# Kernel optimization log

Hardware: AMD Instinct MI355X
Metric: run time of the kernel (lower is better)

Reference implementation:

```python
import jax, jax.numpy as jnp
import numpy as np

B, DIM, H, W = 1, 48, 128, 128
NH = 1  # num_heads; original broadcasting only valid for num_heads == 1


def setup_inputs() -> dict:
    key = jax.random.key(0)
    ks = jax.random.split(key, 5)
    x = jax.random.normal(ks[0], (B, DIM, H, W), jnp.float32)
    # 1x1 conv weights stored as [out, in] matrices (bias=False)
    qkv_w = jax.random.normal(ks[1], (3 * DIM, DIM), jnp.float32) * 0.05
    # depthwise 3x3 conv weight, groups = 3*DIM -> [3*DIM, 1, 3, 3]
    dw_w = jax.random.normal(ks[2], (3 * DIM, 1, 3, 3), jnp.float32) * 0.05
    proj_w = jax.random.normal(ks[3], (DIM, DIM), jnp.float32) * 0.05
    temperature = jnp.ones((NH, 1, 1), jnp.float32)
    return {"x": x, "qkv_w": qkv_w, "dw_w": dw_w, "proj_w": proj_w,
            "temperature": temperature}


def _l2norm(t, eps=1e-12):
    # F.normalize(dim=-1): x / max(||x||_2, eps)
    n = jnp.sqrt(jnp.sum(t * t, axis=-1, keepdims=True))
    return t / jnp.maximum(n, eps)


def reference(x, qkv_w, dw_w, proj_w, temperature):
    b, c, h, w = x.shape
    # qkv 1x1 conv (pointwise) then 3x3 depthwise conv
    qkv = jnp.einsum('bchw,oc->bohw', x, qkv_w)
    qkv = jax.lax.conv_general_dilated(
        qkv, dw_w, window_strides=(1, 1), padding='SAME',
        feature_group_count=3 * c,
        dimension_numbers=('NCHW', 'OIHW', 'NCHW'))
    q, k, v = jnp.split(qkv, 3, axis=1)  # each [b, c, h, w]
    # b c h w -> b (h w) c
    tok = lambda t: t.reshape(b, c, h * w).transpose(0, 2, 1)
    q, k, v = tok(q), tok(k), tok(v)
    q = _l2norm(q)
    k = _l2norm(k)
    # full (hw x hw) cosine attention with learned temperature (scalar, NH=1)
    attn = jnp.einsum('bnc,bmc->bnm', q, k) * temperature  # [b, hw, hw]
    attn = jax.nn.softmax(attn, axis=-1)
    out = jnp.einsum('bnm,bmc->bnc', attn, v)  # [b, hw, c]
    out = out.transpose(0, 2, 1).reshape(b, c, h, w)
    return jnp.einsum('bchw,oc->bohw', out, proj_w)
```

## Files before the change

### kernel.cpp

```cpp
#include <hip/hip_runtime.h>
#include <hip/hip_bf16.h>

#define NPIX 16384
#define NC   48

typedef __attribute__((ext_vector_type(16))) float f32x16;
typedef __attribute__((ext_vector_type(8))) short short8v;
typedef __attribute__((ext_vector_type(8))) unsigned short ushort8v;
typedef __attribute__((ext_vector_type(2))) unsigned int uint2v;

static __device__ __forceinline__ unsigned short f2bf(float x) {
  union { float f; unsigned u; } v; v.f = x;
  unsigned r = v.u + 0x7fffu + ((v.u >> 16) & 1u);
  return (unsigned short)(r >> 16);
}
static __device__ __forceinline__ float bf2f(unsigned short b) {
  union { unsigned u; float f; } v; v.u = ((unsigned)b) << 16;
  return v.f;
}

__global__ __launch_bounds__(256) void k_qkv(const float* __restrict__ in,
                                             const float* __restrict__ w,
                                             unsigned short* __restrict__ out) {
  int p = blockIdx.x * 256 + threadIdx.x;
  int og = blockIdx.y * 16;
  __shared__ float wl[16][NC];
  for (int i = threadIdx.x; i < 16 * NC; i += 256)
    wl[i / NC][i % NC] = w[(og + i / NC) * NC + i % NC];
  __syncthreads();
  float acc[16];
#pragma unroll
  for (int j = 0; j < 16; ++j) acc[j] = 0.f;
  for (int c = 0; c < NC; ++c) {
    float xv = in[c * NPIX + p];
#pragma unroll
    for (int j = 0; j < 16; ++j) acc[j] += xv * wl[j][c];
  }
#pragma unroll
  for (int j = 0; j < 16; ++j) out[(og + j) * NPIX + p] = f2bf(acc[j]);
}

__global__ __launch_bounds__(256) void k_dwconv(const unsigned short* __restrict__ in,
                                                const float* __restrict__ w,
                                                unsigned short* __restrict__ out) {
  __shared__ unsigned short srows[18][136];
  const int o = blockIdx.y;
  const int by = blockIdx.x;
  const int tid = threadIdx.x;
  const float* wt = w + o * 9;
  for (int idx = tid; idx < 288; idx += 256) {
    int r = idx >> 4, cx = idx & 15;
    int gy = by * 16 + r - 1;
    ushort8v vv = {0, 0, 0, 0, 0, 0, 0, 0};
    if (gy >= 0 && gy < 128)
      vv = *(const ushort8v*)(in + o * NPIX + gy * 128 + cx * 8);
    *(ushort8v*)&srows[r][cx * 8] = vv;
  }
  __syncthreads();
  const int r = tid >> 4;
  const int x0 = (tid & 15) * 8;
  float row[3][10];
#pragma unroll
  for (int dy = 0; dy < 3; ++dy) {
    int lr = r + dy;
    ushort8v mid = *(const ushort8v*)&srows[lr][x0];
#pragma unroll
    for (int j = 0; j < 8; ++j) row[dy][j + 1] = bf2f(mid[j]);
    row[dy][0] = (x0 > 0) ? bf2f(srows[lr][x0 - 1]) : 0.f;
    row[dy][9] = (x0 + 8 < 128) ? bf2f(srows[lr][x0 + 8]) : 0.f;
  }
  float wv[9];
#pragma unroll
  for (int i = 0; i < 9; ++i) wv[i] = wt[i];
  unsigned short res[8];
#pragma unroll
  for (int j = 0; j < 8; ++j) {
    float acc = 0.f;
#pragma unroll
    for (int dy = 0; dy < 3; ++dy)
#pragma unroll
      for (int dx = 0; dx < 3; ++dx)
        acc += wv[dy * 3 + dx] * row[dy][j + dx];
    res[j] = f2bf(acc);
  }
  int gy = by * 16 + r;
  *(ushort8v*)(out + o * NPIX + gy * 128 + x0) = *(ushort8v*)res;
}

__global__ __launch_bounds__(128) void k_norm(const unsigned short* __restrict__ dwqb,
                                              const float* __restrict__ temp,
                                              unsigned short* __restrict__ qn,
                                              unsigned short* __restrict__ kn) {
  const int tid = threadIdx.x;
  const int p = blockIdx.x * 64 + (tid & 63);
  const int half = tid >> 6;
  float t = temp[0] * 1.44269504088896f;
  const unsigned short* src = dwqb + half * 48 * NPIX;
  float v[48];
  float sq = 0.f;
#pragma unroll
  for (int c = 0; c < 48; ++c) {
    v[c] = bf2f(src[c * NPIX + p]);
    sq += v[c] * v[c];
  }
  float scale = (half == 0 ? t : 1.f) / fmaxf(sqrtf(sq), 1e-12f);
  unsigned short ob[48];
#pragma unroll
  for (int c = 0; c < 48; ++c) ob[c] = f2bf(v[c] * scale);
  unsigned short* dst = (half == 0 ? qn : kn) + p * 48;
#pragma unroll
  for (int j = 0; j < 6; ++j)
    *(ushort8v*)(dst + j * 8) = *(ushort8v*)&ob[j * 8];
}

__global__ __launch_bounds__(256) void k_attn8(const unsigned short* __restrict__ qn,
                                               const unsigned short* __restrict__ kn,
                                               const unsigned short* __restrict__ vb,
                                               float* __restrict__ numS) {
  __shared__ __align__(16) char smem[57344];
  const int tid = threadIdx.x;
  const int lane = tid & 63, wid = tid >> 6;
  const int l31 = lane & 31, lh = lane >> 5;
  const int bidx = blockIdx.x;
  const int ks = bidx & 7;
  const int qb = bidx >> 3;
  const int qbase = qb * 128 + wid * 32;

  short8v qf[3];
#pragma unroll
  for (int s = 0; s < 3; ++s)
    qf[s] = *(const short8v*)(qn + (qbase + l31) * 48 + s * 16 + lh * 8);

  f32x16 acc[2];
#pragma unroll
  for (int b = 0; b < 2; ++b)
#pragma unroll
    for (int r = 0; r < 16; ++r) acc[b][r] = 0.f;

  int kgoff[3], kloff[3], vgoff[3], vloff[3];
#pragma unroll
  for (int i = 0; i < 3; ++i) {
    int chunk = tid + 256 * i;
    int key = chunk / 6, part = chunk - key * 6;
    kgoff[i] = key * 48 + part * 8;
    kloff[i] = (key * 96 + part * 16) ^ ((key & 7) << 4);
    int c2 = chunk >> 4, kp = chunk & 15;
    vgoff[i] = c2 * NPIX + kp * 8;
    vloff[i] = 12288 + ((c2 * 256 + kp * 16) ^ ((c2 & 15) << 4));
  }

  for (int i = tid; i < 512; i += 256) {
    int b = i >> 8, j = i & 255;
    int c = 48 + (j >> 4), kp = j & 15;
    unsigned short val = (c == 48) ? (unsigned short)0x3F80 : (unsigned short)0;
    ushort8v vv = {val, val, val, val, val, val, val, val};
    *(ushort8v*)(smem + b * 28672 + 12288 + ((c * 256 + kp * 16) ^ ((c & 15) << 4))) = vv;
  }
  {
    const int m0 = ks * 2048;
#pragma unroll
    for (int i = 0; i < 3; ++i) {
      *(short8v*)(smem + kloff[i]) = *(const short8v*)(kn + m0 * 48 + kgoff[i]);
      *(short8v*)(smem + vloff[i]) = *(const short8v*)(vb + m0 + vgoff[i]);
    }
  }
  __syncthreads();

  for (int t = 0; t < 16; ++t) {
    char* buf = smem + (t & 1) * 28672;
    char* nbuf = smem + ((t + 1) & 1) * 28672;
    short8v pfk[3], pfv[3];
    const bool hasNext = (t + 1 < 16);
    if (hasNext) {
      const int m0n = ks * 2048 + (t + 1) * 128;
#pragma unroll
      for (int i = 0; i < 3; ++i) {
        pfk[i] = *(const short8v*)(kn + m0n * 48 + kgoff[i]);
        pfv[i] = *(const short8v*)(vb + m0n + vgoff[i]);
      }
    }
#pragma unroll
    for (int kb = 0; kb < 128; kb += 32) {
      f32x16 sacc;
#pragma unroll
      for (int r = 0; r < 16; ++r) sacc[r] = 0.f;
      int key = kb + l31;
#pragma unroll
      for (int s = 0; s < 3; ++s) {
        short8v kf = *(const short8v*)(buf +
            ((key * 96 + s * 32 + lh * 16) ^ ((key & 7) << 4)));
        sacc = __builtin_amdgcn_mfma_f32_32x32x16_bf16(kf, qf[s], sacc, 0, 0, 0);
      }
      float p[16];
#pragma unroll
      for (int r = 0; r < 16; ++r) p[r] = __builtin_amdgcn_exp2f(sacc[r]);
#pragma unroll
      for (int h = 0; h < 2; ++h) {
        unsigned a0, a1, b0, b1;
        asm("v_cvt_pk_bf16_f32 %0, %1, %2" : "=v"(a0) : "v"(p[8 * h + 0]), "v"(p[8 * h + 1]));
        asm("v_cvt_pk_bf16_f32 %0, %1, %2" : "=v"(a1) : "v"(p[8 * h + 2]), "v"(p[8 * h + 3]));
        asm("v_cvt_pk_bf16_f32 %0, %1, %2" : "=v"(b0) : "v"(p[8 * h + 4]), "v"(p[8 * h + 5]));
        asm("v_cvt_pk_bf16_f32 %0, %1, %2" : "=v"(b1) : "v"(p[8 * h + 6]), "v"(p[8 * h + 7]));
        uint2v s0 = __builtin_amdgcn_permlane32_swap(a0, b0, false, false);
        uint2v s1 = __builtin_amdgcn_permlane32_swap(a1, b1, false, false);
        union { unsigned u[4]; short8v v; } pa;
        pa.u[0] = s0[0]; pa.u[1] = s1[0]; pa.u[2] = s0[1]; pa.u[3] = s1[1];
        int kbase = kb + 16 * h + 8 * lh;
        short8v vf0 = *(const short8v*)(buf + 12288 +
            ((l31 * 256 + kbase * 2) ^ ((l31 & 15) << 4)));
        acc[0] = __builtin_amdgcn_mfma_f32_32x32x16_bf16(pa.v, vf0, acc[0], 0, 0, 0);
        int c1 = 32 + l31;
        short8v vf1 = *(const short8v*)(buf + 12288 +
            ((c1 * 256 + kbase * 2) ^ ((c1 & 15) << 4)));
        acc[1] = __builtin_amdgcn_mfma_f32_32x32x16_bf16(pa.v, vf1, acc[1], 0, 0, 0);
      }
    }
    if (hasNext) {
#pragma unroll
      for (int i = 0; i < 3; ++i) {
        *(short8v*)(nbuf + kloff[i]) = pfk[i];
        *(short8v*)(nbuf + vloff[i]) = pfv[i];
      }
    }
    __syncthreads();
  }

  __syncthreads();
  float* ot = (float*)smem + wid * (32 * 52);
#pragma unroll
  for (int r = 0; r < 16; ++r) {
    int q = (r & 3) + 8 * (r >> 2) + 4 * lh;
    ot[q * 52 + l31] = acc[0][r];
    if (l31 < 17) ot[q * 52 + 32 + l31] = acc[1][r];
  }
  __syncthreads();
  for (int idx = lane; idx < 49 * 32; idx += 64) {
    int q = idx & 31, c = idx >> 5;
    atomicAdd(&numS[(c << 14) + qbase + q], ot[q * 52 + c]);
  }
}

__global__ __launch_bounds__(256) void k_proj(const float* __restrict__ numS,
                                              const float* __restrict__ w,
                                              float* __restrict__ out) {
  __shared__ float wl[48][48];
  __shared__ float tok[48][64];
  __shared__ float dinv[64];
  const int t = threadIdx.x;
  const int px = t & 63, grp = t >> 6;
  const int p0 = blockIdx.x * 64;
  for (int i = t; i < 48 * 48; i += 256) wl[i / 48][i % 48] = w[i];
#pragma unroll
  for (int i = 0; i < 12; ++i) {
    int c = grp * 12 + i;
    tok[c][px] = numS[(c << 14) + p0 + px];
  }
  if (grp == 0) dinv[px] = 1.f / numS[(48 << 14) + p0 + px];
  __syncthreads();
  float rd = dinv[px];
#pragma unroll
  for (int i = 0; i < 12; ++i) {
    int o = grp * 12 + i;
    float a = 0.f;
#pragma unroll
    for (int c = 0; c < 48; ++c) a += wl[o][c] * tok[c][px];
    out[o * NPIX + p0 + px] = a * rd;
  }
}

extern "C" void kernel_launch(void* const* d_in, const int* in_sizes, int n_in,
                              void* d_out, int out_size, void* d_ws, size_t ws_size,
                              hipStream_t stream) {
  const float* x      = (const float*)d_in[0];
  const float* qkv_w  = (const float*)d_in[1];
  const float* dw_w   = (const float*)d_in[2];
  const float* proj_w = (const float*)d_in[3];
  const float* temp   = (const float*)d_in[4];

  char* wsb = (char*)d_ws;
  unsigned short* qn   = (unsigned short*)wsb;
  unsigned short* kn   = (unsigned short*)(wsb + 1572864);
  unsigned short* dwqb = (unsigned short*)(wsb + 3145728);
  unsigned short* vb   = dwqb + 96 * NPIX;
  unsigned short* qkvb = (unsigned short*)(wsb + 7864320);
  float* numS = (float*)(wsb + 7864320);

  k_qkv<<<dim3(64, 9), 256, 0, stream>>>(x, qkv_w, qkvb);
  k_dwconv<<<dim3(8, 144), 256, 0, stream>>>(qkvb, dw_w, dwqb);
  k_norm<<<dim3(256), 128, 0, stream>>>(dwqb, temp, qn, kn);
  hipMemsetAsync(numS, 0, (size_t)49 * NPIX * 4, stream);
  k_attn8<<<dim3(1024), 256, 0, stream>>>(qn, kn, vb, numS);
  k_proj<<<dim3(256), 256, 0, stream>>>(numS, proj_w, (float*)d_out);
}
```

Before: 120.6 us.

## Double attention block to 512 threads so K/V tiles serve 256 queries

The attention kernel now runs 512-thread blocks covering 256 queries (8 waves) instead of 128, with half as many blocks. Each staged K/V tile in shared memory is reused by twice as many query waves, halving global K/V traffic per query. The load work is redistributed so each thread moves three chunks, some from K and some from V. The cost is fewer blocks in flight (512 over the CUs), larger per-block synchronisation, and possibly lower occupancy.

```diff
diff --git a/kernel.cpp b/kernel.cpp
--- a/kernel.cpp
+++ b/kernel.cpp
@@ -113,7 +113,7 @@
     *(ushort8v*)(dst + j * 8) = *(ushort8v*)&ob[j * 8];
 }
 
-__global__ __launch_bounds__(256) void k_attn8(const unsigned short* __restrict__ qn,
+__global__ __launch_bounds__(512) void k_attn8(const unsigned short* __restrict__ qn,
                                                const unsigned short* __restrict__ kn,
                                                const unsigned short* __restrict__ vb,
                                                float* __restrict__ numS) {
@@ -124,7 +124,7 @@
   const int bidx = blockIdx.x;
   const int ks = bidx & 7;
   const int qb = bidx >> 3;
-  const int qbase = qb * 128 + wid * 32;
+  const int qbase = qb * 256 + wid * 32;
 
   short8v qf[3];
 #pragma unroll
@@ -137,20 +137,27 @@
 #pragma unroll
     for (int r = 0; r < 16; ++r) acc[b][r] = 0.f;
 
-  int kgoff[3], kloff[3], vgoff[3], vloff[3];
+  int goff[3], loff[3];
+  bool isK[3];
 #pragma unroll
   for (int i = 0; i < 3; ++i) {
-    int chunk = tid + 256 * i;
-    int key = chunk / 6, part = chunk - key * 6;
-    kgoff[i] = key * 48 + part * 8;
-    kloff[i] = (key * 96 + part * 16) ^ ((key & 7) << 4);
-    int c2 = chunk >> 4, kp = chunk & 15;
-    vgoff[i] = c2 * NPIX + kp * 8;
-    vloff[i] = 12288 + ((c2 * 256 + kp * 16) ^ ((c2 & 15) << 4));
-  }
-
-  for (int i = tid; i < 512; i += 256) {
-    int b = i >> 8, j = i & 255;
+    int chunk = tid + 512 * i;
+    if (chunk < 768) {
+      int key = chunk / 6, part = chunk - key * 6;
+      isK[i] = true;
+      goff[i] = key * 48 + part * 8;
+      loff[i] = (key * 96 + part * 16) ^ ((key & 7) << 4);
+    } else {
+      int cv = chunk - 768;
+      int c2 = cv >> 4, kp = cv & 15;
+      isK[i] = false;
+      goff[i] = c2 * NPIX + kp * 8;
+      loff[i] = 12288 + ((c2 * 256 + kp * 16) ^ ((c2 & 15) << 4));
+    }
+  }
+
+  {
+    int b = tid >> 8, j = tid & 255;
     int c = 48 + (j >> 4), kp = j & 15;
     unsigned short val = (c == 48) ? (unsigned short)0x3F80 : (unsigned short)0;
     ushort8v vv = {val, val, val, val, val, val, val, val};
@@ -160,8 +167,9 @@
     const int m0 = ks * 2048;
 #pragma unroll
     for (int i = 0; i < 3; ++i) {
-      *(short8v*)(smem + kloff[i]) = *(const short8v*)(kn + m0 * 48 + kgoff[i]);
-      *(short8v*)(smem + vloff[i]) = *(const short8v*)(vb + m0 + vgoff[i]);
+      short8v v = isK[i] ? *(const short8v*)(kn + m0 * 48 + goff[i])
+                         : *(const short8v*)(vb + m0 + goff[i]);
+      *(short8v*)(smem + loff[i]) = v;
     }
   }
   __syncthreads();
@@ -169,15 +177,14 @@
   for (int t = 0; t < 16; ++t) {
     char* buf = smem + (t & 1) * 28672;
     char* nbuf = smem + ((t + 1) & 1) * 28672;
-    short8v pfk[3], pfv[3];
+    short8v pf[3];
     const bool hasNext = (t + 1 < 16);
     if (hasNext) {
       const int m0n = ks * 2048 + (t + 1) * 128;
 #pragma unroll
-      for (int i = 0; i < 3; ++i) {
-        pfk[i] = *(const short8v*)(kn + m0n * 48 + kgoff[i]);
-        pfv[i] = *(const short8v*)(vb + m0n + vgoff[i]);
-      }
+      for (int i = 0; i < 3; ++i)
+        pf[i] = isK[i] ? *(const short8v*)(kn + m0n * 48 + goff[i])
+                       : *(const short8v*)(vb + m0n + goff[i]);
     }
 #pragma unroll
     for (int kb = 0; kb < 128; kb += 32) {
@@ -217,10 +224,8 @@
     }
     if (hasNext) {
 #pragma unroll
-      for (int i = 0; i < 3; ++i) {
-        *(short8v*)(nbuf + kloff[i]) = pfk[i];
-        *(short8v*)(nbuf + vloff[i]) = pfv[i];
-      }
+      for (int i = 0; i < 3; ++i)
+        *(short8v*)(nbuf + loff[i]) = pf[i];
     }
     __syncthreads();
   }
@@ -289,6 +294,6 @@
   k_dwconv<<<dim3(8, 144), 256, 0, stream>>>(qkvb, dw_w, dwqb);
   k_norm<<<dim3(256), 128, 0, stream>>>(dwqb, temp, qn, kn);
   hipMemsetAsync(numS, 0, (size_t)49 * NPIX * 4, stream);
-  k_attn8<<<dim3(1024), 256, 0, stream>>>(qn, kn, vb, numS);
+  k_attn8<<<dim3(512), 512, 0, stream>>>(qn, kn, vb, numS);
   k_proj<<<dim3(256), 256, 0, stream>>>(numS, proj_w, (float*)d_out);
 }
```

Result: faster. 111.0 us (median of 2 runs) (-7.9%).
